# Performance work log

Hardware: AMD Instinct MI355X
Metric: run time of the kernel (lower is better)

## Reference

```python
import jax, jax.numpy as jnp
import numpy as np

P, D = 8192, 512


def setup_inputs() -> dict:
    key = jax.random.key(0)
    ks = jax.random.split(key, 8)
    s = 1.0 / np.sqrt(D)
    return {
        "F_chunks": jax.random.normal(ks[0], (P, D), dtype=jnp.float32),
        "Wq": jax.random.normal(ks[1], (D, D), dtype=jnp.float32) * s,
        "bq": jax.random.normal(ks[2], (D,), dtype=jnp.float32) * 0.01,
        "Wk": jax.random.normal(ks[3], (D, D), dtype=jnp.float32) * s,
        "bk": jax.random.normal(ks[4], (D,), dtype=jnp.float32) * 0.01,
        "Wv": jax.random.normal(ks[5], (D, D), dtype=jnp.float32) * s,
        "bv": jax.random.normal(ks[6], (D,), dtype=jnp.float32) * 0.01,
        "lam": jnp.float32(2.0),
    }


def _cdist_l2(x):
    # pairwise Euclidean distance, grad-safe at zero (matches torch.cdist values)
    sq_norm = jnp.sum(x * x, axis=-1)                       # [p]
    sq = sq_norm[:, None] + sq_norm[None, :] - 2.0 * (x @ x.T)  # [p, p]
    sq = jnp.maximum(sq, 0.0)
    safe = jnp.where(sq > 0.0, sq, 1.0)
    return jnp.where(sq > 0.0, jnp.sqrt(safe), 0.0)


def reference(F_chunks, Wq, bq, Wk, bk, Wv, bv, lam):
    p, d = F_chunks.shape
    Q = F_chunks @ Wq.T + bq
    K = F_chunks @ Wk.T + bk
    V = F_chunks @ Wv.T + bv
    logits = (Q @ K.T) * (1.0 / np.sqrt(d))                 # [p, p]
    dist = _cdist_l2(F_chunks)                               # [p, p]
    attn = jax.nn.softmax(logits - lam * dist, axis=-1)      # [p, p]
    F_out = attn @ V                                         # [p, d]
    return (F_out, dist)
```

## Files before the change

kernel.cpp:

```cpp
#include <hip/hip_runtime.h>

#define PP 8192
#define DD 512
#define NJT (PP / 64)
#define NSPLIT 2
#define NJT3 (PP / NSPLIT / 32)

typedef short bf16x8 __attribute__((ext_vector_type(8)));
typedef float f32x4 __attribute__((ext_vector_type(4)));
typedef unsigned short u16;
typedef unsigned int u32;

__device__ __forceinline__ u16 f2bf(float x) {
  u32 u = __float_as_uint(x);
  u += 0x7fffu + ((u >> 16) & 1u);
  return (u16)(u >> 16);
}
__device__ __forceinline__ float bf2f(u16 h) {
  return __uint_as_float(((u32)h) << 16);
}
__device__ __forceinline__ f32x4 mfma_bf16(bf16x8 a, bf16x8 b, f32x4 c) {
  return __builtin_amdgcn_mfma_f32_16x16x32_bf16(a, b, c, 0, 0, 0);
}
__device__ __forceinline__ void gload_lds16(const u16* g, u16* l) {
  __builtin_amdgcn_global_load_lds(
      (const __attribute__((address_space(1))) void*)g,
      (__attribute__((address_space(3))) void*)l, 16, 0, 0);
}

__global__ void prep_wt_kernel(const float* __restrict__ Wq, const float* __restrict__ Wk,
                               const float* __restrict__ Wv, u16* __restrict__ WqT,
                               u16* __restrict__ WkT, u16* __restrict__ Wvb) {
  int i = blockIdx.x * 256 + threadIdx.x;
  int a = i >> 9, k = i & 511;
  WqT[(size_t)k * DD + a] = f2bf(Wq[i]);
  WkT[(size_t)k * DD + a] = f2bf(Wk[i]);
  Wvb[i] = f2bf(Wv[i]);
}

__global__ void kb_kernel(const float* __restrict__ Wk, const float* __restrict__ bq,
                          float* __restrict__ kb) {
  __shared__ float red[8][32];
  int kloc = threadIdx.x & 31, ag = threadIdx.x >> 5;
  int k = blockIdx.x * 32 + kloc;
  float s = 0.f;
  for (int a = ag * 64; a < ag * 64 + 64; ++a) s += bq[a] * Wk[(size_t)a * DD + k];
  red[ag][kloc] = s;
  __syncthreads();
  if (threadIdx.x < 32) {
    float t = 0.f;
#pragma unroll
    for (int g = 0; g < 8; ++g) t += red[g][threadIdx.x];
    kb[blockIdx.x * 32 + threadIdx.x] = t * 0.04419417382415922f;
  }
}

__global__ void prep_f_kernel(const float* __restrict__ F, const float* __restrict__ kb,
                              u16* __restrict__ Fb, float2* __restrict__ nv) {
  int wid = threadIdx.x >> 6, lane = threadIdx.x & 63;
  int row = blockIdx.x * 4 + wid;
  const float* src = F + (size_t)row * DD + lane * 8;
  float4 a = *(const float4*)src;
  float4 b = *(const float4*)(src + 4);
  float v[8] = {a.x, a.y, a.z, a.w, b.x, b.y, b.z, b.w};
  const float* kp = kb + lane * 8;
  float4 ka = *(const float4*)kp;
  float4 kc = *(const float4*)(kp + 4);
  float kw[8] = {ka.x, ka.y, ka.z, ka.w, kc.x, kc.y, kc.z, kc.w};
  u16 h[8];
  float s = 0.f, d = 0.f;
#pragma unroll
  for (int j = 0; j < 8; ++j) {
    h[j] = f2bf(v[j]);
    float f = bf2f(h[j]);
    s += f * f;
    d += f * kw[j];
  }
  u32 pk[4];
#pragma unroll
  for (int j = 0; j < 4; ++j) pk[j] = (u32)h[2 * j] | ((u32)h[2 * j + 1] << 16);
  *(uint4*)(Fb + (size_t)row * DD + lane * 8) = make_uint4(pk[0], pk[1], pk[2], pk[3]);
#pragma unroll
  for (int dd = 1; dd < 64; dd <<= 1) { s += __shfl_xor(s, dd); d += __shfl_xor(d, dd); }
  if (lane == 0) nv[row] = make_float2(s, d);
}

__global__ __launch_bounds__(256) void mt_kernel(const u16* __restrict__ WkT,
                                                 const u16* __restrict__ WqT,
                                                 u16* __restrict__ MT) {
  int lane = threadIdx.x & 63, wm = threadIdx.x >> 6;
  int l15 = lane & 15, lg = lane >> 4;
  int rowA = blockIdx.x * 64 + wm * 16 + l15;
  int rowC0 = blockIdx.x * 64 + wm * 16 + lg * 4;
  int colbase = blockIdx.y * 64;
  f32x4 z = {0.f, 0.f, 0.f, 0.f};
  f32x4 acc[4] = {z, z, z, z};
#pragma unroll
  for (int kk = 0; kk < 16; ++kk) {
    bf16x8 aF = *(const bf16x8*)(WkT + (size_t)rowA * DD + kk * 32 + lg * 8);
#pragma unroll
    for (int nf = 0; nf < 4; ++nf) {
      bf16x8 bW = *(const bf16x8*)(WqT + (size_t)(colbase + nf * 16 + l15) * DD + kk * 32 + lg * 8);
      acc[nf] = mfma_bf16(aF, bW, acc[nf]);
    }
  }
  const float isd = 0.04419417382415922f;
#pragma unroll
  for (int nf = 0; nf < 4; ++nf) {
    int col = colbase + nf * 16 + l15;
#pragma unroll
    for (int r = 0; r < 4; ++r)
      MT[(size_t)(rowC0 + r) * DD + col] = f2bf(acc[nf][r] * isd);
  }
}

__global__ __launch_bounds__(256) void gv_kernel(
    const u16* __restrict__ Fb, const u16* __restrict__ MT, const u16* __restrict__ Wvb,
    const float* __restrict__ bv, u16* __restrict__ G, u16* __restrict__ Vt) {
  int mat = blockIdx.z;
  const u16* W = (mat == 0) ? MT : Wvb;
  int lane = threadIdx.x & 63, wm = threadIdx.x >> 6;
  int l15 = lane & 15, lg = lane >> 4;
  int rowA = blockIdx.x * 64 + wm * 16 + l15;
  int rowC0 = blockIdx.x * 64 + wm * 16 + lg * 4;
  int colbase = blockIdx.y * 64;
  f32x4 z = {0.f, 0.f, 0.f, 0.f};
  f32x4 acc[4] = {z, z, z, z};
#pragma unroll
  for (int kk = 0; kk < 16; ++kk) {
    bf16x8 aF = *(const bf16x8*)(Fb + (size_t)rowA * DD + kk * 32 + lg * 8);
#pragma unroll
    for (int nf = 0; nf < 4; ++nf) {
      bf16x8 bW = *(const bf16x8*)(W + (size_t)(colbase + nf * 16 + l15) * DD + kk * 32 + lg * 8);
      acc[nf] = mfma_bf16(aF, bW, acc[nf]);
    }
  }
#pragma unroll
  for (int nf = 0; nf < 4; ++nf) {
    int col = colbase + nf * 16 + l15;
    if (mat == 1) {
      float bb = bv[col];
      ushort4 vv = make_ushort4(f2bf(acc[nf][0] + bb), f2bf(acc[nf][1] + bb),
                                f2bf(acc[nf][2] + bb), f2bf(acc[nf][3] + bb));
      *(ushort4*)(Vt + (size_t)col * PP + rowC0) = vv;
    } else {
#pragma unroll
      for (int r = 0; r < 4; ++r)
        G[(size_t)(rowC0 + r) * DD + col] = f2bf(acc[nf][r]);
    }
  }
}

__global__ __launch_bounds__(256)
__attribute__((amdgpu_waves_per_eu(2, 4))) void sd3_kernel(
    const u16* __restrict__ G, const u16* __restrict__ Fb,
    const float2* __restrict__ nv, const float* __restrict__ lamp,
    float* __restrict__ Dist, u16* __restrict__ P, float* __restrict__ partial) {
  const float lam = lamp[0];
  int lane = threadIdx.x & 63, wid = threadIdx.x >> 6;
  int wm = wid >> 1, wn = wid & 1;
  int l15 = lane & 15, lg = lane >> 4;
  int rowA = blockIdx.x * 32 + wm * 16 + l15;
  int rowC0 = blockIdx.x * 32 + wm * 16 + lg * 4;
  int kbase = blockIdx.y * (PP / NSPLIT);

  __shared__ u16 Ftile[2][32][DD];

  bf16x8 gf[16], ff[16];
#pragma unroll
  for (int c = 0; c < 16; ++c) {
    gf[c] = *(const bf16x8*)(G + (size_t)rowA * DD + c * 32 + lg * 8);
    ff[c] = *(const bf16x8*)(Fb + (size_t)rowA * DD + c * 32 + lg * 8);
  }
  float ni[4];
#pragma unroll
  for (int r = 0; r < 4; ++r) ni[r] = nv[rowC0 + r].x;
  float rs[4] = {0.f, 0.f, 0.f, 0.f};
  f32x4 z = {0.f, 0.f, 0.f, 0.f};

  int kl = wn * 16 + l15;
  int swz = kl & 7;

#pragma unroll
  for (int t = 0; t < 8; ++t) {
    int row = wid * 8 + t;
    gload_lds16(Fb + (size_t)(kbase + row) * DD + ((lane ^ (row & 7)) * 8),
                &Ftile[0][row][0]);
  }
  __syncthreads();

#pragma unroll 1
  for (int jt = 0; jt < NJT3; ++jt) {
    int key0 = kbase + jt * 32;
    int cur = jt & 1;
    if (jt + 1 < NJT3) {
#pragma unroll
      for (int t = 0; t < 8; ++t) {
        int row = wid * 8 + t;
        gload_lds16(Fb + (size_t)(key0 + 32 + row) * DD + ((lane ^ (row & 7)) * 8),
                    &Ftile[cur ^ 1][row][0]);
      }
    }
    const u16* ft = &Ftile[cur][0][0];
    f32x4 sqk0 = z, sqk1 = z, sff0 = z, sff1 = z;
#pragma unroll
    for (int kk = 0; kk < 16; kk += 2) {
      bf16x8 bF0 = *(const bf16x8*)(ft + (size_t)kl * DD + (((kk * 4 + lg) ^ swz) * 8));
      bf16x8 bF1 = *(const bf16x8*)(ft + (size_t)kl * DD + ((((kk + 1) * 4 + lg) ^ swz) * 8));
      sqk0 = mfma_bf16(gf[kk], bF0, sqk0);
      sff0 = mfma_bf16(ff[kk], bF0, sff0);
      sqk1 = mfma_bf16(gf[kk + 1], bF1, sqk1);
      sff1 = mfma_bf16(ff[kk + 1], bF1, sff1);
    }
    int colB = key0 + kl;
    float2 nvj = nv[colB];
#pragma unroll
    for (int r = 0; r < 4; ++r) {
      float sq = ni[r] + nvj.x - 2.0f * (sff0[r] + sff1[r]);
      sq = fmaxf(sq, 0.f);
      float dist = __builtin_amdgcn_sqrtf(sq);
      Dist[(size_t)(rowC0 + r) * PP + colB] = dist;
      float s = (sqk0[r] + sqk1[r]) + nvj.y - lam * dist;
      float p = __expf(fminf(s, 60.f));
      P[(size_t)(rowC0 + r) * PP + colB] = f2bf(p);
      rs[r] += p;
    }
    __syncthreads();
  }
#pragma unroll
  for (int d = 1; d < 16; d <<= 1) {
#pragma unroll
    for (int r = 0; r < 4; ++r) rs[r] += __shfl_xor(rs[r], d);
  }
  if (l15 == 0) {
#pragma unroll
    for (int r = 0; r < 4; ++r)
      partial[(size_t)(blockIdx.y * 2 + wn) * PP + rowC0 + r] = rs[r];
  }
}

__global__ void rowsum_kernel(const float* __restrict__ partial, float* __restrict__ rowsum) {
  int r = blockIdx.x * 256 + threadIdx.x;
  float s = 0.f;
#pragma unroll
  for (int cb = 0; cb < 4; ++cb) s += partial[(size_t)cb * PP + r];
  rowsum[r] = s;
}

#define KB 128
__global__ __launch_bounds__(256)
__attribute__((amdgpu_waves_per_eu(4, 4))) void pv2_kernel(
    const u16* __restrict__ P, const u16* __restrict__ Vt,
    const float* __restrict__ rowsum, float* __restrict__ Fout) {
  int lane = threadIdx.x & 63, wid = threadIdx.x >> 6;
  int l15 = lane & 15, lg = lane >> 4;
  int q0 = blockIdx.x * 64;
  int col0 = blockIdx.y * 64 + wid * 16;
  __shared__ u16 Pt[2][64][KB];
  f32x4 z = {0.f, 0.f, 0.f, 0.f};
  f32x4 o[4] = {z, z, z, z};

#pragma unroll
  for (int i = 0; i < 4; ++i) {
    int row = wid * 16 + i * 4 + (lane >> 4);
    int g = (lane & 8) | ((lane & 7) ^ (row & 7));
    gload_lds16(P + (size_t)(q0 + row) * PP + g * 8, &Pt[0][wid * 16 + i * 4][0]);
  }
  __syncthreads();

#pragma unroll 1
  for (int kt = 0; kt < PP / KB; ++kt) {
    int cur = kt & 1;
    int k0 = kt * KB;
    bf16x8 aPc[4], bVc;
#pragma unroll
    for (int qf = 0; qf < 4; ++qf) {
      int row = qf * 16 + l15;
      int s0 = lg;
      int gp = (s0 & 8) | ((s0 & 7) ^ (row & 7));
      aPc[qf] = *(const bf16x8*)(&Pt[cur][row][0] + gp * 8);
    }
    bVc = *(const bf16x8*)(Vt + (size_t)(col0 + l15) * PP + k0 + lg * 8);
    if (kt + 1 < PP / KB) {
      int k0n = (kt + 1) * KB;
#pragma unroll
      for (int i = 0; i < 4; ++i) {
        int row = wid * 16 + i * 4 + (lane >> 4);
        int g = (lane & 8) | ((lane & 7) ^ (row & 7));
        gload_lds16(P + (size_t)(q0 + row) * PP + k0n + g * 8,
                    &Pt[cur ^ 1][wid * 16 + i * 4][0]);
      }
    }
#pragma unroll
    for (int kc = 0; kc < KB / 32; ++kc) {
      bf16x8 aPn[4], bVn;
      if (kc + 1 < KB / 32) {
        int sn = (kc + 1) * 4 + lg;
#pragma unroll
        for (int qf = 0; qf < 4; ++qf) {
          int row = qf * 16 + l15;
          int gp = (sn & 8) | ((sn & 7) ^ (row & 7));
          aPn[qf] = *(const bf16x8*)(&Pt[cur][row][0] + gp * 8);
        }
        bVn = *(const bf16x8*)(Vt + (size_t)(col0 + l15) * PP + k0 + (kc + 1) * 32 + lg * 8);
      }
#pragma unroll
      for (int qf = 0; qf < 4; ++qf) o[qf] = mfma_bf16(aPc[qf], bVc, o[qf]);
      if (kc + 1 < KB / 32) {
#pragma unroll
        for (int qf = 0; qf < 4; ++qf) aPc[qf] = aPn[qf];
        bVc = bVn;
      }
    }
    __syncthreads();
  }
  float inv[4][4];
#pragma unroll
  for (int qf = 0; qf < 4; ++qf)
#pragma unroll
    for (int r = 0; r < 4; ++r)
      inv[qf][r] = 1.0f / rowsum[q0 + qf * 16 + lg * 4 + r];
#pragma unroll
  for (int qf = 0; qf < 4; ++qf) {
#pragma unroll
    for (int r = 0; r < 4; ++r)
      Fout[(size_t)(q0 + qf * 16 + lg * 4 + r) * DD + col0 + l15] = o[qf][r] * inv[qf][r];
  }
}

__global__ __launch_bounds__(512)
__attribute__((amdgpu_waves_per_eu(2, 2))) void fused_kernel(
    const u16* __restrict__ G, const u16* __restrict__ Fb, const u16* __restrict__ Vt,
    const float2* __restrict__ nv, const float* __restrict__ lamp,
    float* __restrict__ out) {
  float* Fout = out;
  float* Dist = out + (size_t)PP * DD;
  const float lam = lamp[0];
  int lane = threadIdx.x & 63, wid = threadIdx.x >> 6;
  int wm = wid >> 2, wn = wid & 3;
  int l15 = lane & 15, lg = lane >> 4;
  int rowA = blockIdx.x * 32 + wm * 16 + l15;
  int rowC0 = blockIdx.x * 32 + wm * 16 + lg * 4;

  __shared__ u16 Ftile[2][64][DD];
  __shared__ u16 P_lds[32][72];
  __shared__ float redmax[8][16];
  __shared__ float redsum[8][16];

  bf16x8 gf[16], ff[16];
#pragma unroll
  for (int c = 0; c < 16; ++c) {
    gf[c] = *(const bf16x8*)(G + (size_t)rowA * DD + c * 32 + lg * 8);
    ff[c] = *(const bf16x8*)(Fb + (size_t)rowA * DD + c * 32 + lg * 8);
  }
  float ni[4];
#pragma unroll
  for (int r = 0; r < 4; ++r) ni[r] = nv[rowC0 + r].x;
  float m_run[2][4], l_run[2][4];
#pragma unroll
  for (int g = 0; g < 2; ++g)
#pragma unroll
    for (int r = 0; r < 4; ++r) { m_run[g][r] = -1e30f; l_run[g][r] = 0.f; }
  f32x4 z = {0.f, 0.f, 0.f, 0.f};
  f32x4 o[8] = {z, z, z, z, z, z, z, z};

  int kl = wn * 16 + l15;
  int swz = kl & 7;
  int col0 = wid * 64;

#pragma unroll
  for (int t = 0; t < 8; ++t) {
    int row = wid * 8 + t;
    gload_lds16(Fb + (size_t)row * DD + ((lane ^ (row & 7)) * 8), &Ftile[0][row][0]);
  }
  __syncthreads();

#pragma unroll 1
  for (int jt = 0; jt < NJT; ++jt) {
    int key0 = jt * 64;
    int cur = jt & 1;
    if (jt + 1 < NJT) {
      int nb = cur ^ 1;
#pragma unroll
      for (int t = 0; t < 8; ++t) {
        int row = wid * 8 + t;
        gload_lds16(Fb + (size_t)(key0 + 64 + row) * DD + ((lane ^ (row & 7)) * 8),
                    &Ftile[nb][row][0]);
      }
    }
    const u16* ft = &Ftile[cur][0][0];
    f32x4 sqk = z, sff = z;
#pragma unroll
    for (int kk = 0; kk < 16; ++kk) {
      bf16x8 bF = *(const bf16x8*)(ft + (size_t)kl * DD + (((kk * 4 + lg) ^ swz) * 8));
      sqk = mfma_bf16(gf[kk], bF, sqk);
      sff = mfma_bf16(ff[kk], bF, sff);
    }
    int colB = key0 + kl;
    float2 nvj = nv[colB];
    float pv[4], tmax[4];
#pragma unroll
    for (int r = 0; r < 4; ++r) {
      float sq = ni[r] + nvj.x - 2.0f * sff[r];
      sq = fmaxf(sq, 0.f);
      float dist = sqrtf(sq);
      Dist[(size_t)(rowC0 + r) * PP + colB] = dist;
      float s = sqk[r] + nvj.y - lam * dist;
      pv[r] = s;
      tmax[r] = s;
    }
#pragma unroll
    for (int d = 1; d < 16; d <<= 1) {
#pragma unroll
      for (int r = 0; r < 4; ++r) tmax[r] = fmaxf(tmax[r], __shfl_xor(tmax[r], d));
    }
    if (l15 == 0) {
#pragma unroll
      for (int r = 0; r < 4; ++r) redmax[wid][lg * 4 + r] = tmax[r];
    }
    __syncthreads();
    float mnew[2][4], alpha[2][4];
#pragma unroll
    for (int g = 0; g < 2; ++g) {
#pragma unroll
      for (int r = 0; r < 4; ++r) {
        float mt = m_run[g][r];
#pragma unroll
        for (int ow = 0; ow < 4; ++ow) mt = fmaxf(mt, redmax[g * 4 + ow][lg * 4 + r]);
        mnew[g][r] = mt;
        alpha[g][r] = __expf(m_run[g][r] - mt);
      }
    }
    float tsum[4];
#pragma unroll
    for (int r = 0; r < 4; ++r) {
      float mo = (wm == 0) ? mnew[0][r] : mnew[1][r];
      pv[r] = __expf(pv[r] - mo);
      tsum[r] = pv[r];
    }
#pragma unroll
    for (int d = 1; d < 16; d <<= 1) {
#pragma unroll
      for (int r = 0; r < 4; ++r) tsum[r] += __shfl_xor(tsum[r], d);
    }
#pragma unroll
    for (int r = 0; r < 4; ++r)
      P_lds[wm * 16 + lg * 4 + r][wn * 16 + l15] = f2bf(pv[r]);
    if (l15 == 0) {
#pragma unroll
      for (int r = 0; r < 4; ++r) redsum[wid][lg * 4 + r] = tsum[r];
    }
    __syncthreads();
#pragma unroll
    for (int g = 0; g < 2; ++g) {
#pragma unroll
      for (int r = 0; r < 4; ++r) {
        float s4 = 0.f;
#pragma unroll
        for (int ow = 0; ow < 4; ++ow) s4 += redsum[g * 4 + ow][lg * 4 + r];
        l_run[g][r] = l_run[g][r] * alpha[g][r] + s4;
        m_run[g][r] = mnew[g][r];
      }
    }
#pragma unroll
    for (int g = 0; g < 2; ++g) {
#pragma unroll
      for (int nt = 0; nt < 4; ++nt) {
#pragma unroll
        for (int r = 0; r < 4; ++r) o[g * 4 + nt][r] *= alpha[g][r];
      }
    }
#pragma unroll
    for (int kc = 0; kc < 2; ++kc) {
      bf16x8 aP0 = *(const bf16x8*)(&P_lds[l15][kc * 32 + lg * 8]);
      bf16x8 aP1 = *(const bf16x8*)(&P_lds[16 + l15][kc * 32 + lg * 8]);
#pragma unroll
      for (int nt = 0; nt < 4; ++nt) {
        int n = col0 + nt * 16 + l15;
        bf16x8 bV = *(const bf16x8*)(Vt + (size_t)n * PP + key0 + kc * 32 + lg * 8);
        o[nt] = mfma_bf16(aP0, bV, o[nt]);
        o[4 + nt] = mfma_bf16(aP1, bV, o[4 + nt]);
      }
    }
  }
  float inv[2][4];
#pragma unroll
  for (int g = 0; g < 2; ++g)
#pragma unroll
    for (int r = 0; r < 4; ++r) inv[g][r] = 1.0f / l_run[g][r];
#pragma unroll
  for (int g = 0; g < 2; ++g) {
#pragma unroll
    for (int nt = 0; nt < 4; ++nt) {
#pragma unroll
      for (int r = 0; r < 4; ++r)
        Fout[(size_t)(blockIdx.x * 32 + g * 16 + lg * 4 + r) * DD + col0 + nt * 16 + l15] =
            o[g * 4 + nt][r] * inv[g][r];
    }
  }
}

extern "C" void kernel_launch(void* const* d_in, const int* in_sizes, int n_in,
                              void* d_out, int out_size, void* d_ws, size_t ws_size,
                              hipStream_t stream) {
  const float* F   = (const float*)d_in[0];
  const float* Wq  = (const float*)d_in[1];
  const float* bq  = (const float*)d_in[2];
  const float* Wk  = (const float*)d_in[3];
  const float* bk  = (const float*)d_in[4];
  const float* Wv  = (const float*)d_in[5];
  const float* bv  = (const float*)d_in[6];
  const float* lam = (const float*)d_in[7];
  float* out = (float*)d_out;
  (void)bk;

  u16* ws  = (u16*)d_ws;
  u16* Fb  = ws;
  u16* G   = Fb + (size_t)PP * DD;
  u16* Vt  = G + (size_t)PP * DD;
  u16* WqT = Vt + (size_t)PP * DD;
  u16* WkT = WqT + (size_t)DD * DD;
  u16* Wvb = WkT + (size_t)DD * DD;
  u16* MT  = Wvb + (size_t)DD * DD;
  float2* nv = (float2*)(MT + (size_t)DD * DD);
  float* kb  = (float*)(nv + PP);
  u16* P        = (u16*)(kb + DD);
  float* partial = (float*)(P + (size_t)PP * PP);
  float* rowsum  = partial + (size_t)4 * PP;
  size_t need = (size_t)((char*)(rowsum + PP) - (char*)d_ws);

  prep_wt_kernel<<<1024, 256, 0, stream>>>(Wq, Wk, Wv, WqT, WkT, Wvb);
  kb_kernel<<<16, 256, 0, stream>>>(Wk, bq, kb);
  prep_f_kernel<<<PP / 4, 256, 0, stream>>>(F, kb, Fb, nv);
  mt_kernel<<<dim3(8, 8), 256, 0, stream>>>(WkT, WqT, MT);
  gv_kernel<<<dim3(PP / 64, DD / 64, 2), 256, 0, stream>>>(Fb, MT, Wvb, bv, G, Vt);

  if (ws_size >= need) {
    float* Dist = out + (size_t)PP * DD;
    sd3_kernel<<<dim3(PP / 32, NSPLIT), 256, 0, stream>>>(G, Fb, nv, lam, Dist, P, partial);
    rowsum_kernel<<<PP / 256, 256, 0, stream>>>(partial, rowsum);
    pv2_kernel<<<dim3(PP / 64, 8), 256, 0, stream>>>(P, Vt, rowsum, out);
  } else {
    fused_kernel<<<PP / 32, 512, 0, stream>>>(G, Fb, Vt, nv, lam, out);
  }
}
```

Before: 483.9 us.

## Fuse P·V into score kernel via LDS tile, drop P matrix round-trip

The score/distance kernel now keeps each 32x32 bf16 probability tile in LDS and immediately multiplies it by V (read straight from global memory), accumulating per-split partial outputs in registers. The separate pv2 kernel and the 8192x8192 bf16 P buffer in workspace are replaced by a small merge kernel that adds the two split partials and normalizes by the row sum. This removes writing and rereading about 128MB of P. In exchange it adds 64 accumulator registers per lane, uncached V reads per key tile from every block, and an extra fp32 partial-output pass.

Measured after the change: 888.6 us. +83.6%, slower.

```diff
diff --git a/kernel.cpp b/kernel.cpp
--- a/kernel.cpp
+++ b/kernel.cpp
@@ -152,10 +152,10 @@
 }
 
 __global__ __launch_bounds__(256)
-__attribute__((amdgpu_waves_per_eu(2, 4))) void sd3_kernel(
-    const u16* __restrict__ G, const u16* __restrict__ Fb,
+__attribute__((amdgpu_waves_per_eu(2, 4))) void sdpv_kernel(
+    const u16* __restrict__ G, const u16* __restrict__ Fb, const u16* __restrict__ Vt,
     const float2* __restrict__ nv, const float* __restrict__ lamp,
-    float* __restrict__ Dist, u16* __restrict__ P, float* __restrict__ partial) {
+    float* __restrict__ Dist, float* __restrict__ Opart, float* __restrict__ partial) {
   const float lam = lamp[0];
   int lane = threadIdx.x & 63, wid = threadIdx.x >> 6;
   int wm = wid >> 1, wn = wid & 1;
@@ -165,6 +165,7 @@
   int kbase = blockIdx.y * (PP / NSPLIT);
 
   __shared__ u16 Ftile[2][32][DD];
+  __shared__ u16 P_lds[2][32][36];
 
   bf16x8 gf[16], ff[16];
 #pragma unroll
@@ -177,9 +178,13 @@
   for (int r = 0; r < 4; ++r) ni[r] = nv[rowC0 + r].x;
   float rs[4] = {0.f, 0.f, 0.f, 0.f};
   f32x4 z = {0.f, 0.f, 0.f, 0.f};
+  f32x4 o[16];
+#pragma unroll
+  for (int i = 0; i < 16; ++i) o[i] = z;
 
   int kl = wn * 16 + l15;
   int swz = kl & 7;
+  int col0 = wid * 128;
 
 #pragma unroll
   for (int t = 0; t < 8; ++t) {
@@ -222,10 +227,20 @@
       Dist[(size_t)(rowC0 + r) * PP + colB] = dist;
       float s = (sqk0[r] + sqk1[r]) + nvj.y - lam * dist;
       float p = __expf(fminf(s, 60.f));
-      P[(size_t)(rowC0 + r) * PP + colB] = f2bf(p);
+      P_lds[cur][wm * 16 + lg * 4 + r][wn * 16 + l15] = f2bf(p);
       rs[r] += p;
     }
     __syncthreads();
+
+    bf16x8 aP0 = *(const bf16x8*)(&P_lds[cur][l15][lg * 8]);
+    bf16x8 aP1 = *(const bf16x8*)(&P_lds[cur][16 + l15][lg * 8]);
+#pragma unroll
+    for (int nt = 0; nt < 8; ++nt) {
+      int n = col0 + nt * 16 + l15;
+      bf16x8 bV = *(const bf16x8*)(Vt + (size_t)n * PP + key0 + lg * 8);
+      o[nt] = mfma_bf16(aP0, bV, o[nt]);
+      o[8 + nt] = mfma_bf16(aP1, bV, o[8 + nt]);
+    }
   }
 #pragma unroll
   for (int d = 1; d < 16; d <<= 1) {
@@ -236,6 +251,17 @@
 #pragma unroll
     for (int r = 0; r < 4; ++r)
       partial[(size_t)(blockIdx.y * 2 + wn) * PP + rowC0 + r] = rs[r];
+  }
+  float* Od = Opart + (size_t)blockIdx.y * PP * DD;
+#pragma unroll
+  for (int g = 0; g < 2; ++g) {
+#pragma unroll
+    for (int nt = 0; nt < 8; ++nt) {
+#pragma unroll
+      for (int r = 0; r < 4; ++r)
+        Od[(size_t)(blockIdx.x * 32 + g * 16 + lg * 4 + r) * DD + col0 + nt * 16 + l15] =
+            o[g * 8 + nt][r];
+    }
   }
 }
 
@@ -247,85 +273,20 @@
   rowsum[r] = s;
 }
 
-#define KB 128
-__global__ __launch_bounds__(256)
-__attribute__((amdgpu_waves_per_eu(4, 4))) void pv2_kernel(
-    const u16* __restrict__ P, const u16* __restrict__ Vt,
-    const float* __restrict__ rowsum, float* __restrict__ Fout) {
-  int lane = threadIdx.x & 63, wid = threadIdx.x >> 6;
-  int l15 = lane & 15, lg = lane >> 4;
-  int q0 = blockIdx.x * 64;
-  int col0 = blockIdx.y * 64 + wid * 16;
-  __shared__ u16 Pt[2][64][KB];
-  f32x4 z = {0.f, 0.f, 0.f, 0.f};
-  f32x4 o[4] = {z, z, z, z};
-
-#pragma unroll
-  for (int i = 0; i < 4; ++i) {
-    int row = wid * 16 + i * 4 + (lane >> 4);
-    int g = (lane & 8) | ((lane & 7) ^ (row & 7));
-    gload_lds16(P + (size_t)(q0 + row) * PP + g * 8, &Pt[0][wid * 16 + i * 4][0]);
-  }
-  __syncthreads();
-
-#pragma unroll 1
-  for (int kt = 0; kt < PP / KB; ++kt) {
-    int cur = kt & 1;
-    int k0 = kt * KB;
-    bf16x8 aPc[4], bVc;
-#pragma unroll
-    for (int qf = 0; qf < 4; ++qf) {
-      int row = qf * 16 + l15;
-      int s0 = lg;
-      int gp = (s0 & 8) | ((s0 & 7) ^ (row & 7));
-      aPc[qf] = *(const bf16x8*)(&Pt[cur][row][0] + gp * 8);
-    }
-    bVc = *(const bf16x8*)(Vt + (size_t)(col0 + l15) * PP + k0 + lg * 8);
-    if (kt + 1 < PP / KB) {
-      int k0n = (kt + 1) * KB;
-#pragma unroll
-      for (int i = 0; i < 4; ++i) {
-        int row = wid * 16 + i * 4 + (lane >> 4);
-        int g = (lane & 8) | ((lane & 7) ^ (row & 7));
-        gload_lds16(P + (size_t)(q0 + row) * PP + k0n + g * 8,
-                    &Pt[cur ^ 1][wid * 16 + i * 4][0]);
-      }
-    }
-#pragma unroll
-    for (int kc = 0; kc < KB / 32; ++kc) {
-      bf16x8 aPn[4], bVn;
-      if (kc + 1 < KB / 32) {
-        int sn = (kc + 1) * 4 + lg;
-#pragma unroll
-        for (int qf = 0; qf < 4; ++qf) {
-          int row = qf * 16 + l15;
-          int gp = (sn & 8) | ((sn & 7) ^ (row & 7));
-          aPn[qf] = *(const bf16x8*)(&Pt[cur][row][0] + gp * 8);
-        }
-        bVn = *(const bf16x8*)(Vt + (size_t)(col0 + l15) * PP + k0 + (kc + 1) * 32 + lg * 8);
-      }
-#pragma unroll
-      for (int qf = 0; qf < 4; ++qf) o[qf] = mfma_bf16(aPc[qf], bVc, o[qf]);
-      if (kc + 1 < KB / 32) {
-#pragma unroll
-        for (int qf = 0; qf < 4; ++qf) aPc[qf] = aPn[qf];
-        bVc = bVn;
-      }
-    }
-    __syncthreads();
-  }
-  float inv[4][4];
-#pragma unroll
-  for (int qf = 0; qf < 4; ++qf)
-#pragma unroll
-    for (int r = 0; r < 4; ++r)
-      inv[qf][r] = 1.0f / rowsum[q0 + qf * 16 + lg * 4 + r];
-#pragma unroll
-  for (int qf = 0; qf < 4; ++qf) {
-#pragma unroll
-    for (int r = 0; r < 4; ++r)
-      Fout[(size_t)(q0 + qf * 16 + lg * 4 + r) * DD + col0 + l15] = o[qf][r] * inv[qf][r];
-  }
+__global__ __launch_bounds__(256) void merge_kernel(const float* __restrict__ Opart,
+                                                    const float* __restrict__ rowsum,
+                                                    float* __restrict__ Fout) {
+  int i = blockIdx.x * 256 + threadIdx.x;
+  int row = i >> 7;
+  int c = (i & 127) * 4;
+  float inv = 1.0f / rowsum[row];
+  float4 a = *(const float4*)(Opart + (size_t)row * DD + c);
+  float4 b = *(const float4*)(Opart + (size_t)PP * DD + (size_t)row * DD + c);
+  a.x = (a.x + b.x) * inv;
+  a.y = (a.y + b.y) * inv;
+  a.z = (a.z + b.z) * inv;
+  a.w = (a.w + b.w) * inv;
+  *(float4*)(Fout + (size_t)row * DD + c) = a;
 }
 
 __global__ __launch_bounds__(512)
@@ -524,8 +485,8 @@
   u16* MT  = Wvb + (size_t)DD * DD;
   float2* nv = (float2*)(MT + (size_t)DD * DD);
   float* kb  = (float*)(nv + PP);
-  u16* P        = (u16*)(kb + DD);
-  float* partial = (float*)(P + (size_t)PP * PP);
+  float* Opart   = (float*)(kb + DD);
+  float* partial = Opart + (size_t)2 * PP * DD;
   float* rowsum  = partial + (size_t)4 * PP;
   size_t need = (size_t)((char*)(rowsum + PP) - (char*)d_ws);
 
@@ -537,9 +498,10 @@
 
   if (ws_size >= need) {
     float* Dist = out + (size_t)PP * DD;
-    sd3_kernel<<<dim3(PP / 32, NSPLIT), 256, 0, stream>>>(G, Fb, nv, lam, Dist, P, partial);
+    sdpv_kernel<<<dim3(PP / 32, NSPLIT), 256, 0, stream>>>(G, Fb, Vt, nv, lam, Dist, Opart,
+                                                           partial);
     rowsum_kernel<<<PP / 256, 256, 0, stream>>>(partial, rowsum);
-    pv2_kernel<<<dim3(PP / 64, 8), 256, 0, stream>>>(P, Vt, rowsum, out);
+    merge_kernel<<<PP * DD / 4 / 256, 256, 0, stream>>>(Opart, rowsum, out);
   } else {
     fused_kernel<<<PP / 32, 512, 0, stream>>>(G, Fb, Vt, nv, lam, out);
   }
```
